# Kernel tuning notes

Hardware: AMD Instinct MI355X
Metric: run time of the kernel (lower is better)

The kernel has to match this reference:

```python
import jax, jax.numpy as jnp
import numpy as np

N_NODES = 100_000
N_EDGES = 3_200_000
VOCAB = 128          # in_dim (node token vocabulary)
HID = 128            # hidden_dim == out_dim
HEADS = 8            # n_heads; jaccard kernel uses HEADS//2 score heads
POS = 8              # pos_enc_dim
N_CLASSES = 7
TOPK_FACTOR = 3
K = int(np.ceil(8 * TOPK_FACTOR * N_NODES / 3000))  # = 800, per source formula


def setup_inputs() -> dict:
    key = jax.random.key(0)
    ks = jax.random.split(key, 16)
    inp = {
        'h_tokens': jax.random.randint(ks[0], (N_NODES,), 0, VOCAB),
        'src': jax.random.randint(ks[1], (N_EDGES,), 0, N_NODES),
        'dst': jax.random.randint(ks[2], (N_EDGES,), 0, N_NODES),
        'e': jax.random.uniform(ks[3], (N_EDGES,), dtype=jnp.float32),  # per-edge jaccard similarity
        'h_lap_pos_enc': jax.random.normal(ks[4], (N_NODES, POS), dtype=jnp.float32),
        # learned params
        'emb': jax.random.normal(ks[5], (VOCAB, HID), dtype=jnp.float32) * 0.02,
        'lap_W': jax.random.normal(ks[6], (POS, HID), dtype=jnp.float32) * 0.02,
        'lap_b': jnp.zeros((HID,), dtype=jnp.float32),
        'W0': jax.random.normal(ks[7], (HID, HID // 2), dtype=jnp.float32) * 0.05,
        'b0': jnp.zeros((HID // 2,), dtype=jnp.float32),
        'W1': jax.random.normal(ks[8], (HID // 2, HID // 4), dtype=jnp.float32) * 0.05,
        'b1': jnp.zeros((HID // 4,), dtype=jnp.float32),
        'W2': jax.random.normal(ks[9], (HID // 4, N_CLASSES), dtype=jnp.float32) * 0.05,
        'b2': jnp.zeros((N_CLASSES,), dtype=jnp.float32),
    }
    return inp


def reference(h_tokens, src, dst, e, h_lap_pos_enc, emb, lap_W, lap_b,
              W0, b0, W1, b1, W2, b2):
    # --- node embedding + laplacian positional encoding ---
    h = emb[h_tokens] + (h_lap_pos_enc @ lap_W + lap_b)          # [N, HID]

    # --- initialize_edge_score: score = 1 / in_degree(dst), per score-head ---
    ones_e = jnp.ones_like(e)
    in_deg = jax.ops.segment_sum(ones_e, dst, num_segments=N_NODES)  # [N] float
    deg_safe = jnp.maximum(in_deg, 1.0)
    score = jnp.broadcast_to((1.0 / deg_safe)[dst][:, None, None],
                             (e.shape[0], HEADS // 2, 1))          # [E, H/2, 1]

    # --- jaccard_sparse_metric: per-dst max(mailbox) - mean(mailbox) - log(in_degree) ---
    seg_max = jax.ops.segment_max(e, dst, num_segments=N_NODES)     # [N]
    seg_mean = jax.ops.segment_sum(e, dst, num_segments=N_NODES) / deg_safe
    jaccard_M = jnp.where(in_deg > 0,
                          seg_max - seg_mean - jnp.log(deg_safe),
                          -jnp.inf)                                 # [N]

    # --- top-k node selection for subgraph sparsification ---
    _, top_idx = jax.lax.top_k(jaccard_M, K)                        # [K] node ids

    # LiteGTLayer stack is external to the provided source; treated as identity here.

    # --- MLPReadout ---
    x = jax.nn.relu(h @ W0 + b0)
    x = jax.nn.relu(x @ W1 + b1)
    h_out = x @ W2 + b2                                             # [N, n_classes]
    return h_out, score, jaccard_M, top_idx
```

## Files before the change

### kernel.cpp

```cpp
#include <hip/hip_runtime.h>
#include <math.h>

#define N_NODES 100000
#define N_EDGES 3200000
#define KSEL    800
#define CANDCAP 4096
#define SLOTS   128
#define NBUCK   196
#define BUCKCAP 18432
#define EPB     8192
#define PARTB   391
#define PREB    18
#define GATB    3125
#define MLPB    1563

#define OUT_SCORE 700000
#define OUT_JACC  13500000
#define OUT_TOP   13600000

#define OFF_GCUR     0
#define OFF_GH1      1024
#define OFF_GH2      9216
#define OFF_CCUR     263168
#define OFF_SCAL     279552
#define ZERO_END     279808
#define OFF_CANDID   279808
#define OFF_RCP      679808
#define OFF_DEG      1079808
#define OFF_KEYS     1479808
#define OFF_CANDNODE 2279808
#define OFF_CANDKEY  2296192
#define OFF_CEDGE    2328960
#define OFF_PART     4426112
#define OFF_E1       18876800
#define OFF_L1       18909568
#define OFF_C1       18911616

__global__ __launch_bounds__(512) void k_part(
    const int* __restrict__ dst, const float* __restrict__ e,
    unsigned int* __restrict__ gcur, unsigned int* __restrict__ partbuf,
    const float* __restrict__ emb, const float* __restrict__ W0,
    const float* __restrict__ lapW, const float* __restrict__ lapb,
    const float* __restrict__ b0,
    float* __restrict__ E1, float* __restrict__ L1, float* __restrict__ c1)
{
    __shared__ unsigned int scnt[256], sexc[256], sgb[256], scur[256];
    __shared__ unsigned int sdata[EPB];
    __shared__ unsigned char sbuck[EPB];

    int sid = blockIdx.x;
    int t = threadIdx.x;

    if (sid >= PARTB) {
        int id = (sid - PARTB) * 512 + t;
        if (id < 8192) {
            int v = id >> 6, c = id & 63;
            float a = 0.f;
            for (int k = 0; k < 128; ++k) a += emb[v * 128 + k] * W0[k * 64 + c];
            E1[id] = a;
        } else if (id < 8704) {
            int r = id - 8192;
            int j = r >> 6, c = r & 63;
            float a = 0.f;
            for (int k = 0; k < 128; ++k) a += lapW[j * 128 + k] * W0[k * 64 + c];
            L1[r] = a;
        } else if (id < 8768) {
            int c = id - 8704;
            float a = b0[c];
            for (int k = 0; k < 128; ++k) a += lapb[k] * W0[k * 64 + c];
            c1[c] = a;
        }
        return;
    }

    long base = (long)sid * EPB;
    int nedge = (int)(N_EDGES - base); if (nedge > EPB) nedge = EPB;
    int myoff = t * 16;
    bool act = myoff < nedge;
    unsigned int pb[16]; unsigned int bb[16];

    if (t < 256) scnt[t] = 0;
    __syncthreads();

    if (act) {
#pragma unroll
        for (int g = 0; g < 4; ++g) {
            int4 d4 = *(const int4*)(dst + base + myoff + g * 4);
            float4 e4 = *(const float4*)(e + base + myoff + g * 4);
            int dd[4] = {d4.x, d4.y, d4.z, d4.w};
            float ee[4] = {e4.x, e4.y, e4.z, e4.w};
#pragma unroll
            for (int j = 0; j < 4; ++j) {
                unsigned int q = (unsigned int)(ee[j] * 65536.0f);
                if (q > 65535u) q = 65535u;
                int idx = g * 4 + j;
                bb[idx] = ((unsigned int)dd[j]) >> 9;
                pb[idx] = (q << 9) | ((unsigned int)dd[j] & 511u);
                atomicAdd(&scnt[bb[idx]], 1u);
            }
        }
    }
    __syncthreads();

    if (t < 64) {
        unsigned int c0 = scnt[t * 4], c1v = scnt[t * 4 + 1];
        unsigned int c2 = scnt[t * 4 + 2], c3 = scnt[t * 4 + 3];
        unsigned int p0 = c0, p1 = p0 + c1v, p2 = p1 + c2, p3 = p2 + c3;
        unsigned int run = p3;
#pragma unroll
        for (int off = 1; off < 64; off <<= 1) {
            unsigned int v = __shfl_up(run, off);
            if (t >= off) run += v;
        }
        unsigned int exc = run - p3;
        sexc[t * 4]     = exc;
        sexc[t * 4 + 1] = exc + p0;
        sexc[t * 4 + 2] = exc + p1;
        sexc[t * 4 + 3] = exc + p2;
    }
    __syncthreads();
    if (t < 256) {
        unsigned int c = scnt[t];
        scur[t] = sexc[t];
        sgb[t] = (c > 0) ? atomicAdd(&gcur[t], c) : 0u;
    }
    __syncthreads();

    if (act) {
#pragma unroll
        for (int j = 0; j < 16; ++j) {
            unsigned int slot = atomicAdd(&scur[bb[j]], 1u);
            sdata[slot] = pb[j];
            sbuck[slot] = (unsigned char)bb[j];
        }
    }
    __syncthreads();

    for (int j = t; j < nedge; j += 512) {
        unsigned int p = sdata[j];
        unsigned int bk = sbuck[j];
        unsigned int gi = sgb[bk] + ((unsigned int)j - sexc[bk]);
        if (gi < BUCKCAP) partbuf[bk * BUCKCAP + gi] = p;
    }
}

__global__ __launch_bounds__(256) void k_bstats(
    const unsigned int* __restrict__ partbuf, const unsigned int* __restrict__ gcur,
    float* __restrict__ out_jacc, float* __restrict__ rcp,
    int* __restrict__ deg_arr, unsigned long long* __restrict__ keys,
    unsigned int* __restrict__ gh1)
{
    __shared__ unsigned int scnt[512];
    __shared__ unsigned int ssum[512];
    __shared__ unsigned int smax[512];
    __shared__ unsigned int lh1[2048];
    int b = blockIdx.x, t = threadIdx.x;
    scnt[t] = 0; scnt[t + 256] = 0;
    ssum[t] = 0; ssum[t + 256] = 0;
    smax[t] = 0; smax[t + 256] = 0;
#pragma unroll
    for (int i = 0; i < 8; ++i) lh1[t + i * 256] = 0;
    __syncthreads();

    unsigned int cnt = gcur[b]; if (cnt > BUCKCAP) cnt = BUCKCAP;
    const unsigned int* pb = partbuf + b * BUCKCAP;
    for (unsigned int i = t; i < cnt; i += 256) {
        unsigned int p = pb[i];
        unsigned int nl = p & 511u;
        unsigned int q = p >> 9;
        atomicAdd(&scnt[nl], 1u);
        atomicAdd(&ssum[nl], q);
        atomicMax(&smax[nl], q);
    }
    __syncthreads();

    for (int tl = t; tl < 512; tl += 256) {
        int node = (b << 9) + tl;
        if (node >= N_NODES) break;
        int d = (int)scnt[tl];
        float jac, r;
        if (d == 0) {
            jac = -INFINITY; r = 1.0f;
        } else {
            float dd = (float)d;
            r = 1.0f / dd;
            float sum = (float)ssum[tl] * (1.0f / 65536.0f);
            float maxf = (float)smax[tl] * (1.0f / 65536.0f);
            float mean = sum / dd;
            float lg = (float)log((double)d);
            jac = (maxf - mean) - lg;
        }
        out_jacc[node] = jac;
        rcp[node] = r;
        deg_arr[node] = d;
        unsigned int s = __float_as_uint(jac);
        unsigned int asc = (s & 0x80000000u) ? ~s : (s | 0x80000000u);
        unsigned int desc = ~asc;
        keys[node] = ((unsigned long long)desc << 32) | (unsigned int)node;
        atomicAdd(&lh1[desc >> 21], 1u);
    }
    __syncthreads();

#pragma unroll
    for (int i = 0; i < 8; ++i) {
        unsigned int c = lh1[t + i * 256];
        if (c) atomicAdd(&gh1[t + i * 256], c);
    }
}

__device__ __forceinline__ void derive_cut1(const unsigned int* gh1,
                                            unsigned int* part,
                                            unsigned int* res,
                                            int t) {
    unsigned int s = 0;
    if (t < 256) {
        for (int b8 = t * 8; b8 < t * 8 + 8; ++b8) s += gh1[b8];
        part[t] = s;
    }
    __syncthreads();
    for (int off = 1; off < 256; off <<= 1) {
        unsigned int v = 0;
        if (t < 256 && t >= off) v = part[t - off];
        __syncthreads();
        if (t < 256) part[t] += v;
        __syncthreads();
    }
    if (t < 256) {
        unsigned int inc = part[t];
        unsigned int base = inc - s;
        if (base < KSEL && inc >= KSEL) {
            unsigned int run = base;
            for (int b8 = t * 8; b8 < t * 8 + 8; ++b8) {
                unsigned int h = gh1[b8];
                if (run + h >= KSEL) { res[0] = (unsigned int)b8; res[1] = run; break; }
                run += h;
            }
        }
    }
    __syncthreads();
}

__global__ __launch_bounds__(1024) void k_hist2(const unsigned long long* __restrict__ keys,
                                                const unsigned int* __restrict__ gh1,
                                                unsigned int* __restrict__ gh2) {
    __shared__ unsigned int part[256];
    __shared__ unsigned int res[2];
    __shared__ unsigned int lh[256];
    int t = threadIdx.x;
    if (t < 256) lh[t] = 0;
    derive_cut1(gh1, part, res, t);
    unsigned int cb11 = res[0];
    int n = blockIdx.x * 1024 + t;
    if (n < N_NODES) {
        unsigned int desc = (unsigned int)(keys[n] >> 32);
        if ((desc >> 21) == cb11)
            atomicAdd(&lh[(desc >> 13) & 255u], 1u);
    }
    __syncthreads();
    if (t < 256 && lh[t]) atomicAdd(&gh2[t], lh[t]);
}

__global__ __launch_bounds__(1024) void k_collect(
    const unsigned long long* __restrict__ keys,
    const unsigned int* __restrict__ gh1, const unsigned int* __restrict__ gh2,
    int* __restrict__ scal,
    int* __restrict__ candid, int* __restrict__ candNode) {
    __shared__ unsigned int part[256];
    __shared__ unsigned int res[2];
    __shared__ unsigned int h2[256];
    __shared__ unsigned int thr_s;
    __shared__ unsigned int wcnt[16], wbase[16], bbase;
    int t = threadIdx.x;
    if (t < 256) h2[t] = gh2[t];
    derive_cut1(gh1, part, res, t);
    if (t == 0) {
        unsigned int run = res[1];
        unsigned int cb8 = 255;
        for (int b8 = 0; b8 < 256; ++b8) {
            run += h2[b8];
            if (run >= KSEL) { cb8 = (unsigned int)b8; break; }
        }
        unsigned long long thr = ((unsigned long long)res[0] << 21)
                               + (((unsigned long long)cb8 + 2ULL) << 13);
        if (thr > 0x100000000ULL) thr = 0x100000000ULL;
        thr_s = (unsigned int)(thr - 1ULL);
    }
    __syncthreads();

    int wv = t >> 6, lane = t & 63;
    int n = blockIdx.x * 1024 + t;
    unsigned int thr = thr_s;
    bool isc = false;
    if (n < N_NODES) {
        unsigned int desc = (unsigned int)(keys[n] >> 32);
        isc = (desc <= thr);
    }
    unsigned long long bal = __ballot(isc);
    if (lane == 0) wcnt[wv] = (unsigned int)__popcll(bal);
    __syncthreads();
    if (t == 0) {
        unsigned int s = 0;
        for (int i = 0; i < 16; ++i) { wbase[i] = s; s += wcnt[i]; }
        bbase = s ? (unsigned int)atomicAdd(&scal[1], (int)s) : 0u;
    }
    __syncthreads();
    if (n < N_NODES) {
        int cid = -1;
        if (isc) {
            unsigned int pos = bbase + wbase[wv]
                             + (unsigned int)__popcll(bal & ((1ULL << lane) - 1ULL));
            if (pos < CANDCAP) {
                cid = (int)pos;
                candNode[pos] = n;
            }
        }
        candid[n] = cid;
    }
}

__global__ __launch_bounds__(512) void k_gather_mlp(
    const int* __restrict__ dst, const float* __restrict__ rcp,
    const int* __restrict__ candid,
    int* __restrict__ ccur, int* __restrict__ cedge,
    float4* __restrict__ out_s,
    const int* __restrict__ tok, const float* __restrict__ pos,
    const float* __restrict__ E1, const float* __restrict__ L1,
    const float* __restrict__ c1,
    const float* __restrict__ W1, const float* __restrict__ b1,
    const float* __restrict__ W2, const float* __restrict__ b2,
    float* __restrict__ out)
{
    int b = blockIdx.x;
    int t = threadIdx.x;

    long i = ((long)b * 512 + t) * 2;
    int2 d2 = *(const int2*)(dst + i);
    float r0 = rcp[d2.x], r1 = rcp[d2.y];
    out_s[i]     = make_float4(r0, r0, r0, r0);
    out_s[i + 1] = make_float4(r1, r1, r1, r1);
    int cc0 = candid[d2.x];
    if (cc0 >= 0) {
        int p = atomicAdd(&ccur[cc0], 1);
        if (p < SLOTS) cedge[cc0 * SLOTS + p] = (int)i;
    }
    int cc1 = candid[d2.y];
    if (cc1 >= 0) {
        int p = atomicAdd(&ccur[cc1], 1);
        if (p < SLOTS) cedge[cc1 * SLOTS + p] = (int)i + 1;
    }

    if (t >= 64 || b >= MLPB) return;
    int node = b * 64 + t;
    if (node >= N_NODES) return;

    int tk = tok[node];
    const float4* p4 = (const float4*)(pos + (long)node * 8);
    float4 pA = p4[0], pB = p4[1];
    float p[8] = {pA.x, pA.y, pA.z, pA.w, pB.x, pB.y, pB.z, pB.w};

    float a2[32];
#pragma unroll
    for (int j = 0; j < 32; ++j) a2[j] = b1[j];

    const float* e1r = E1 + tk * 64;
#pragma unroll 1
    for (int c8 = 0; c8 < 8; ++c8) {
        float4 eA = *(const float4*)(e1r + c8 * 8);
        float4 eB = *(const float4*)(e1r + c8 * 8 + 4);
        float ev[8] = {eA.x, eA.y, eA.z, eA.w, eB.x, eB.y, eB.z, eB.w};
#pragma unroll
        for (int cc = 0; cc < 8; ++cc) {
            int c = c8 * 8 + cc;
            float a = c1[c] + ev[cc];
#pragma unroll
            for (int j = 0; j < 8; ++j) a += p[j] * L1[j * 64 + c];
            float x = fmaxf(a, 0.f);
#pragma unroll
            for (int j = 0; j < 32; ++j)
                a2[j] += x * W1[c * 32 + j];
        }
    }

    float a3[7];
#pragma unroll
    for (int c = 0; c < 7; ++c) a3[c] = b2[c];
#pragma unroll
    for (int k = 0; k < 32; ++k) {
        float xk = fmaxf(a2[k], 0.f);
#pragma unroll
        for (int c = 0; c < 7; ++c)
            a3[c] += xk * W2[k * 7 + c];
    }
    float* op = out + (long)node * 7;
#pragma unroll
    for (int c = 0; c < 7; ++c) op[c] = a3[c];
}

__global__ __launch_bounds__(256) void k_exact(
    const int* __restrict__ dst, const float* __restrict__ e,
    const int* __restrict__ deg_arr,
    const int* __restrict__ candNode,
    const int* __restrict__ cedge, const int* __restrict__ scal,
    float* __restrict__ out_jacc, unsigned long long* __restrict__ candKey) {
    int w = threadIdx.x >> 6;
    int lane = threadIdx.x & 63;
    int cc = scal[1]; if (cc > CANDCAP) cc = CANDCAP;
    int cid = blockIdx.x * 4 + w;
    if (cid >= cc) return;
    int n = candNode[cid];
    int d = deg_arr[n];
    float jac;
    if (d == 0) {
        jac = -INFINITY;
    } else {
        float sum = 0.f, mxv = -INFINITY;
        if (d <= SLOTS) {
            const int* base = cedge + cid * SLOTS;
            int j;
            int i0, i1; float f0, f1;
            j = lane;      i0 = (j < d) ? base[j] : 0x7fffffff; f0 = (j < d) ? e[i0] : 0.f;
            j = 64 + lane; i1 = (j < d) ? base[j] : 0x7fffffff; f1 = (j < d) ? e[i1] : 0.f;
            int last = -1;
            for (int r = 0; r < d; ++r) {
                int mi = 0x7fffffff; float mv = 0.f;
                if (i0 > last && i0 < mi) { mi = i0; mv = f0; }
                if (i1 > last && i1 < mi) { mi = i1; mv = f1; }
#pragma unroll
                for (int s = 32; s >= 1; s >>= 1) {
                    int oi = __shfl_xor(mi, s);
                    float ov = __shfl_xor(mv, s);
                    if (oi < mi) { mi = oi; mv = ov; }
                }
                sum += mv;
                mxv = fmaxf(mxv, mv);
                last = mi;
            }
        } else {
            for (int b0 = 0; b0 < N_EDGES; b0 += 64) {
                int ii = b0 + lane;
                bool m = (ii < N_EDGES) && (dst[ii] == n);
                float v = m ? e[ii] : 0.f;
                unsigned long long bal = __ballot(m);
                while (bal) {
                    int bb = __ffsll(bal) - 1;
                    float hv = __shfl(v, bb);
                    sum += hv;
                    mxv = fmaxf(mxv, hv);
                    bal &= bal - 1;
                }
            }
        }
        float dd = (float)d;
        float mean = sum / dd;
        float lg = (float)log((double)d);
        jac = (mxv - mean) - lg;
    }
    if (lane == 0) {
        out_jacc[n] = jac;
        unsigned int s = __float_as_uint(jac);
        unsigned int asc = (s & 0x80000000u) ? ~s : (s | 0x80000000u);
        candKey[cid] = ((unsigned long long)(~asc) << 32) | (unsigned int)n;
    }
}

__global__ __launch_bounds__(1024) void k_sort(const unsigned long long* __restrict__ candKey,
                                               const int* __restrict__ scal,
                                               float* __restrict__ out_top) {
    __shared__ unsigned long long sk[CANDCAP];
    int t = threadIdx.x;
    int cc = scal[1]; if (cc > CANDCAP) cc = CANDCAP;
    int m = 1024; while (m < cc) m <<= 1;
    for (int i = t; i < m; i += 1024)
        sk[i] = (i < cc) ? candKey[i] : 0xFFFFFFFFFFFFFFFFULL;
    __syncthreads();
    for (int k = 2; k <= m; k <<= 1) {
        for (int j = k >> 1; j > 0; j >>= 1) {
            for (int i = t; i < m; i += 1024) {
                int ixj = i ^ j;
                if (ixj > i) {
                    unsigned long long a = sk[i], bv = sk[ixj];
                    bool up = ((i & k) == 0);
                    if ((a > bv) == up) { sk[i] = bv; sk[ixj] = a; }
                }
            }
            __syncthreads();
        }
    }
    for (int r = t; r < KSEL; r += 1024)
        out_top[r] = (float)(unsigned int)(sk[r] & 0xFFFFFFFFULL);
}

extern "C" void kernel_launch(void* const* d_in, const int* in_sizes, int n_in,
                              void* d_out, int out_size, void* d_ws, size_t ws_size,
                              hipStream_t stream) {
    const int*   h_tokens = (const int*)d_in[0];
    const int*   dst      = (const int*)d_in[2];
    const float* e        = (const float*)d_in[3];
    const float* pos      = (const float*)d_in[4];
    const float* emb      = (const float*)d_in[5];
    const float* lapW     = (const float*)d_in[6];
    const float* lapb     = (const float*)d_in[7];
    const float* W0 = (const float*)d_in[8];
    const float* b0 = (const float*)d_in[9];
    const float* W1 = (const float*)d_in[10];
    const float* b1 = (const float*)d_in[11];
    const float* W2 = (const float*)d_in[12];
    const float* b2 = (const float*)d_in[13];
    float* out = (float*)d_out;

    char* ws = (char*)d_ws;
    unsigned int* gcur = (unsigned int*)(ws + OFF_GCUR);
    unsigned int* gh1  = (unsigned int*)(ws + OFF_GH1);
    unsigned int* gh2  = (unsigned int*)(ws + OFF_GH2);
    int* ccur = (int*)(ws + OFF_CCUR);
    int* scal = (int*)(ws + OFF_SCAL);
    int* candid = (int*)(ws + OFF_CANDID);
    float* rcp = (float*)(ws + OFF_RCP);
    int* deg_arr = (int*)(ws + OFF_DEG);
    unsigned long long* keys = (unsigned long long*)(ws + OFF_KEYS);
    int* candNode = (int*)(ws + OFF_CANDNODE);
    unsigned long long* candKey = (unsigned long long*)(ws + OFF_CANDKEY);
    int* cedge = (int*)(ws + OFF_CEDGE);
    unsigned int* partbuf = (unsigned int*)(ws + OFF_PART);
    float* E1 = (float*)(ws + OFF_E1);
    float* L1 = (float*)(ws + OFF_L1);
    float* c1 = (float*)(ws + OFF_C1);

    hipMemsetAsync(ws, 0, ZERO_END, stream);

    k_part<<<PARTB + PREB, 512, 0, stream>>>(dst, e, gcur, partbuf,
                                             emb, W0, lapW, lapb, b0, E1, L1, c1);
    k_bstats<<<NBUCK, 256, 0, stream>>>(partbuf, gcur, out + OUT_JACC, rcp,
                                        deg_arr, keys, gh1);
    k_hist2<<<98, 1024, 0, stream>>>(keys, gh1, gh2);
    k_collect<<<98, 1024, 0, stream>>>(keys, gh1, gh2, scal, candid, candNode);
    k_gather_mlp<<<GATB, 512, 0, stream>>>(dst, rcp, candid, ccur, cedge,
                                           (float4*)(out + OUT_SCORE),
                                           h_tokens, pos, E1, L1, c1,
                                           W1, b1, W2, b2, out);
    k_exact<<<1024, 256, 0, stream>>>(dst, e, deg_arr, candNode, cedge, scal,
                                      out + OUT_JACC, candKey);
    k_sort<<<1, 1024, 0, stream>>>(candKey, scal, out + OUT_TOP);
}
```

Baseline: 133.1 us.

## Move node MLP into bucket-stats kernel and widen edge gather to four edges per thread

```diff
diff --git a/kernel.cpp b/kernel.cpp
--- a/kernel.cpp
+++ b/kernel.cpp
@@ -11,8 +11,8 @@
 #define EPB     8192
 #define PARTB   391
 #define PREB    18
-#define GATB    3125
-#define MLPB    1563
+#define MLPNB   391
+#define GATB    1563
 
 #define OUT_SCORE 700000
 #define OUT_JACC  13500000
@@ -148,13 +148,67 @@
     const unsigned int* __restrict__ partbuf, const unsigned int* __restrict__ gcur,
     float* __restrict__ out_jacc, float* __restrict__ rcp,
     int* __restrict__ deg_arr, unsigned long long* __restrict__ keys,
-    unsigned int* __restrict__ gh1)
+    unsigned int* __restrict__ gh1,
+    const int* __restrict__ tok, const float* __restrict__ pos,
+    const float* __restrict__ E1, const float* __restrict__ L1,
+    const float* __restrict__ c1,
+    const float* __restrict__ W1, const float* __restrict__ b1,
+    const float* __restrict__ W2, const float* __restrict__ b2,
+    float* __restrict__ out)
 {
     __shared__ unsigned int scnt[512];
     __shared__ unsigned int ssum[512];
     __shared__ unsigned int smax[512];
     __shared__ unsigned int lh1[2048];
     int b = blockIdx.x, t = threadIdx.x;
+
+    if (b >= NBUCK) {
+        int node = (b - NBUCK) * 256 + t;
+        if (node >= N_NODES) return;
+        int tk = tok[node];
+        const float4* p4 = (const float4*)(pos + (long)node * 8);
+        float4 pA = p4[0], pB = p4[1];
+        float p[8] = {pA.x, pA.y, pA.z, pA.w, pB.x, pB.y, pB.z, pB.w};
+
+        float a2[32];
+#pragma unroll
+        for (int j = 0; j < 32; ++j) a2[j] = b1[j];
+
+        const float* e1r = E1 + tk * 64;
+#pragma unroll 1
+        for (int c8 = 0; c8 < 8; ++c8) {
+            float4 eA = *(const float4*)(e1r + c8 * 8);
+            float4 eB = *(const float4*)(e1r + c8 * 8 + 4);
+            float ev[8] = {eA.x, eA.y, eA.z, eA.w, eB.x, eB.y, eB.z, eB.w};
+#pragma unroll
+            for (int cc = 0; cc < 8; ++cc) {
+                int c = c8 * 8 + cc;
+                float a = c1[c] + ev[cc];
+#pragma unroll
+                for (int j = 0; j < 8; ++j) a += p[j] * L1[j * 64 + c];
+                float x = fmaxf(a, 0.f);
+#pragma unroll
+                for (int j = 0; j < 32; ++j)
+                    a2[j] += x * W1[c * 32 + j];
+            }
+        }
+
+        float a3[7];
+#pragma unroll
+        for (int c = 0; c < 7; ++c) a3[c] = b2[c];
+#pragma unroll
+        for (int k = 0; k < 32; ++k) {
+            float xk = fmaxf(a2[k], 0.f);
+#pragma unroll
+            for (int c = 0; c < 7; ++c)
+                a3[c] += xk * W2[k * 7 + c];
+        }
+        float* op = out + (long)node * 7;
+#pragma unroll
+        for (int c = 0; c < 7; ++c) op[c] = a3[c];
+        return;
+    }
+
     scnt[t] = 0; scnt[t + 256] = 0;
     ssum[t] = 0; ssum[t + 256] = 0;
     smax[t] = 0; smax[t + 256] = 0;
@@ -318,82 +372,40 @@
     }
 }
 
-__global__ __launch_bounds__(512) void k_gather_mlp(
+__global__ __launch_bounds__(512) void k_gather(
     const int* __restrict__ dst, const float* __restrict__ rcp,
     const int* __restrict__ candid,
     int* __restrict__ ccur, int* __restrict__ cedge,
-    float4* __restrict__ out_s,
-    const int* __restrict__ tok, const float* __restrict__ pos,
-    const float* __restrict__ E1, const float* __restrict__ L1,
-    const float* __restrict__ c1,
-    const float* __restrict__ W1, const float* __restrict__ b1,
-    const float* __restrict__ W2, const float* __restrict__ b2,
-    float* __restrict__ out)
+    float4* __restrict__ out_s)
 {
-    int b = blockIdx.x;
-    int t = threadIdx.x;
-
-    long i = ((long)b * 512 + t) * 2;
-    int2 d2 = *(const int2*)(dst + i);
-    float r0 = rcp[d2.x], r1 = rcp[d2.y];
+    long i = ((long)blockIdx.x * 512 + threadIdx.x) * 4;
+    if (i >= N_EDGES) return;
+    int4 d4 = *(const int4*)(dst + i);
+    float r0 = rcp[d4.x], r1 = rcp[d4.y], r2 = rcp[d4.z], r3 = rcp[d4.w];
     out_s[i]     = make_float4(r0, r0, r0, r0);
     out_s[i + 1] = make_float4(r1, r1, r1, r1);
-    int cc0 = candid[d2.x];
-    if (cc0 >= 0) {
-        int p = atomicAdd(&ccur[cc0], 1);
-        if (p < SLOTS) cedge[cc0 * SLOTS + p] = (int)i;
-    }
-    int cc1 = candid[d2.y];
-    if (cc1 >= 0) {
-        int p = atomicAdd(&ccur[cc1], 1);
-        if (p < SLOTS) cedge[cc1 * SLOTS + p] = (int)i + 1;
-    }
-
-    if (t >= 64 || b >= MLPB) return;
-    int node = b * 64 + t;
-    if (node >= N_NODES) return;
-
-    int tk = tok[node];
-    const float4* p4 = (const float4*)(pos + (long)node * 8);
-    float4 pA = p4[0], pB = p4[1];
-    float p[8] = {pA.x, pA.y, pA.z, pA.w, pB.x, pB.y, pB.z, pB.w};
-
-    float a2[32];
-#pragma unroll
-    for (int j = 0; j < 32; ++j) a2[j] = b1[j];
-
-    const float* e1r = E1 + tk * 64;
-#pragma unroll 1
-    for (int c8 = 0; c8 < 8; ++c8) {
-        float4 eA = *(const float4*)(e1r + c8 * 8);
-        float4 eB = *(const float4*)(e1r + c8 * 8 + 4);
-        float ev[8] = {eA.x, eA.y, eA.z, eA.w, eB.x, eB.y, eB.z, eB.w};
-#pragma unroll
-        for (int cc = 0; cc < 8; ++cc) {
-            int c = c8 * 8 + cc;
-            float a = c1[c] + ev[cc];
-#pragma unroll
-            for (int j = 0; j < 8; ++j) a += p[j] * L1[j * 64 + c];
-            float x = fmaxf(a, 0.f);
-#pragma unroll
-            for (int j = 0; j < 32; ++j)
-                a2[j] += x * W1[c * 32 + j];
-        }
-    }
-
-    float a3[7];
-#pragma unroll
-    for (int c = 0; c < 7; ++c) a3[c] = b2[c];
-#pragma unroll
-    for (int k = 0; k < 32; ++k) {
-        float xk = fmaxf(a2[k], 0.f);
-#pragma unroll
-        for (int c = 0; c < 7; ++c)
-            a3[c] += xk * W2[k * 7 + c];
-    }
-    float* op = out + (long)node * 7;
-#pragma unroll
-    for (int c = 0; c < 7; ++c) op[c] = a3[c];
+    out_s[i + 2] = make_float4(r2, r2, r2, r2);
+    out_s[i + 3] = make_float4(r3, r3, r3, r3);
+    int c0 = candid[d4.x];
+    if (c0 >= 0) {
+        int p = atomicAdd(&ccur[c0], 1);
+        if (p < SLOTS) cedge[c0 * SLOTS + p] = (int)i;
+    }
+    int c1 = candid[d4.y];
+    if (c1 >= 0) {
+        int p = atomicAdd(&ccur[c1], 1);
+        if (p < SLOTS) cedge[c1 * SLOTS + p] = (int)i + 1;
+    }
+    int c2 = candid[d4.z];
+    if (c2 >= 0) {
+        int p = atomicAdd(&ccur[c2], 1);
+        if (p < SLOTS) cedge[c2 * SLOTS + p] = (int)i + 2;
+    }
+    int c3 = candid[d4.w];
+    if (c3 >= 0) {
+        int p = atomicAdd(&ccur[c3], 1);
+        if (p < SLOTS) cedge[c3 * SLOTS + p] = (int)i + 3;
+    }
 }
 
 __global__ __launch_bounds__(256) void k_exact(
@@ -530,14 +542,14 @@
 
     k_part<<<PARTB + PREB, 512, 0, stream>>>(dst, e, gcur, partbuf,
                                              emb, W0, lapW, lapb, b0, E1, L1, c1);
-    k_bstats<<<NBUCK, 256, 0, stream>>>(partbuf, gcur, out + OUT_JACC, rcp,
-                                        deg_arr, keys, gh1);
+    k_bstats<<<NBUCK + MLPNB, 256, 0, stream>>>(partbuf, gcur, out + OUT_JACC, rcp,
+                                                deg_arr, keys, gh1,
+                                                h_tokens, pos, E1, L1, c1,
+                                                W1, b1, W2, b2, out);
     k_hist2<<<98, 1024, 0, stream>>>(keys, gh1, gh2);
     k_collect<<<98, 1024, 0, stream>>>(keys, gh1, gh2, scal, candid, candNode);
-    k_gather_mlp<<<GATB, 512, 0, stream>>>(dst, rcp, candid, ccur, cedge,
-                                           (float4*)(out + OUT_SCORE),
-                                           h_tokens, pos, E1, L1, c1,
-                                           W1, b1, W2, b2, out);
+    k_gather<<<GATB, 512, 0, stream>>>(dst, rcp, candid, ccur, cedge,
+                                       (float4*)(out + OUT_SCORE));
     k_exact<<<1024, 256, 0, stream>>>(dst, e, deg_arr, candNode, cedge, scal,
                                       out + OUT_JACC, candKey);
     k_sort<<<1, 1024, 0, stream>>>(candKey, scal, out + OUT_TOP);
```

After: 139.3 us. +4.7%, slower.
